# Optimization experiments

Hardware: AMD Instinct MI355X
Metric: run time of the kernel (lower is better)

The kernel has to match this reference:

```python
import jax, jax.numpy as jnp
import numpy as np

D_ENC, D_PRED, D_JOINT, VOCAB = 512, 640, 640, 1024

def setup_inputs() -> dict:
    key = jax.random.key(0)
    ks = jax.random.split(key, 8)
    B, T, U = 8, 200, 50
    s_enc = 1.0 / np.sqrt(D_ENC)
    s_pred = 1.0 / np.sqrt(D_PRED)
    s_joint = 1.0 / np.sqrt(D_JOINT)
    return {
        "encoder_out": jax.random.normal(ks[0], (B, T, D_ENC), jnp.float32),
        "predictor_out": jax.random.normal(ks[1], (B, U, D_PRED), jnp.float32),
        # nn.Linear weights: (out, in), uniform(-1/sqrt(in), 1/sqrt(in))
        "W_enc": jax.random.uniform(ks[2], (D_JOINT, D_ENC), jnp.float32, -s_enc, s_enc),
        "b_enc": jax.random.uniform(ks[3], (D_JOINT,), jnp.float32, -s_enc, s_enc),
        "W_pred": jax.random.uniform(ks[4], (D_JOINT, D_PRED), jnp.float32, -s_pred, s_pred),
        "b_pred": jax.random.uniform(ks[5], (D_JOINT,), jnp.float32, -s_pred, s_pred),
        "W_out": jax.random.uniform(ks[6], (VOCAB, D_JOINT), jnp.float32, -s_joint, s_joint),
        "b_out": jax.random.uniform(ks[7], (VOCAB,), jnp.float32, -s_joint, s_joint),
    }

def reference(encoder_out, predictor_out, W_enc, b_enc, W_pred, b_pred, W_out, b_out):
    # (B,T,d_joint) and (B,U,d_joint) projections
    enc = jnp.einsum('btd,jd->btj', encoder_out, W_enc) + b_enc
    pred = jnp.einsum('bud,jd->buj', predictor_out, W_pred) + b_pred
    # broadcast-add over (T,U), tanh, then output projection -> (B,T,U,V)
    joint = jnp.tanh(enc[:, :, None, :] + pred[:, None, :, :])
    return jnp.einsum('btuj,vj->btuv', joint, W_out) + b_out
```

## Files before the change

kernel.cpp:

```cpp
#include <hip/hip_runtime.h>
#include <hip/hip_bf16.h>
#include <stdint.h>
#include <stddef.h>

#define D_ENC 512
#define D_J   640
#define VOCAB 1024
#define BB    8
#define TT    200
#define UU    50

typedef __bf16 bf16x8 __attribute__((ext_vector_type(8)));
typedef float  f32x4  __attribute__((ext_vector_type(4)));

static __device__ __forceinline__ unsigned f2bf(float x) {
    union { float f; unsigned u; } v; v.f = x;
    unsigned r = v.u + 0x7FFFu + ((v.u >> 16) & 1u);
    return r >> 16;
}
static __device__ __forceinline__ unsigned pk2(float a, float b) {
    return f2bf(a) | (f2bf(b) << 16);
}

static __device__ __forceinline__ float tanh_fast(float x) {
    float ax = __builtin_fabsf(x);
    float e  = __expf(-2.0f * ax);
    float t  = (1.0f - e) * __builtin_amdgcn_rcpf(1.0f + e);
    return __builtin_copysignf(t, x);
}

__global__ void wcvt_kernel(const float* __restrict__ src,
                            unsigned short* __restrict__ dst, int n8) {
    int i = blockIdx.x * blockDim.x + threadIdx.x;
    if (i >= n8) return;
    const float4* s = (const float4*)src + (size_t)i * 2;
    float4 a = s[0], b = s[1];
    uint4 o;
    o.x = pk2(a.x, a.y); o.y = pk2(a.z, a.w);
    o.z = pk2(b.x, b.y); o.w = pk2(b.z, b.w);
    ((uint4*)dst)[i] = o;
}

__global__ void proj_gemm(const float* __restrict__ A, const float* __restrict__ W,
                          const float* __restrict__ bias, float* __restrict__ C,
                          int M, int K) {
    __shared__ __align__(16) unsigned short Alds[64 * 72];
    __shared__ __align__(16) unsigned short Blds[64 * 72];
    const int tid  = threadIdx.x;
    const int lane = tid & 63, w = tid >> 6;
    const int l15  = lane & 15, quad = lane >> 4;
    const int m0 = blockIdx.x * 64, n0 = blockIdx.y * 64;
    const int srow = tid >> 2, sq = tid & 3;

    f32x4 acc[4];
#pragma unroll
    for (int i = 0; i < 4; ++i) acc[i] = (f32x4){0.f, 0.f, 0.f, 0.f};

    const int am = m0 + srow;
    const float* arow = A + (size_t)am * K + sq * 16;
    const float* wrow = W + (size_t)(n0 + srow) * K + sq * 16;
    unsigned short* adst = &Alds[srow * 72 + sq * 16];
    unsigned short* bdst = &Blds[srow * 72 + sq * 16];

    for (int k0 = 0; k0 < K; k0 += 64) {
        uint4 wa0, wa1;
        if (am < M) {
            const float4* p = (const float4*)(arow + k0);
            float4 x0 = p[0], x1 = p[1], x2 = p[2], x3 = p[3];
            wa0.x = pk2(x0.x, x0.y); wa0.y = pk2(x0.z, x0.w);
            wa0.z = pk2(x1.x, x1.y); wa0.w = pk2(x1.z, x1.w);
            wa1.x = pk2(x2.x, x2.y); wa1.y = pk2(x2.z, x2.w);
            wa1.z = pk2(x3.x, x3.y); wa1.w = pk2(x3.z, x3.w);
        } else {
            wa0 = make_uint4(0u, 0u, 0u, 0u); wa1 = wa0;
        }
        uint4 wb0, wb1;
        {
            const float4* p = (const float4*)(wrow + k0);
            float4 x0 = p[0], x1 = p[1], x2 = p[2], x3 = p[3];
            wb0.x = pk2(x0.x, x0.y); wb0.y = pk2(x0.z, x0.w);
            wb0.z = pk2(x1.x, x1.y); wb0.w = pk2(x1.z, x1.w);
            wb1.x = pk2(x2.x, x2.y); wb1.y = pk2(x2.z, x2.w);
            wb1.z = pk2(x3.x, x3.y); wb1.w = pk2(x3.z, x3.w);
        }
        *(uint4*)adst = wa0; *(uint4*)(adst + 8) = wa1;
        *(uint4*)bdst = wb0; *(uint4*)(bdst + 8) = wb1;
        __syncthreads();
#pragma unroll
        for (int ks = 0; ks < 2; ++ks) {
            bf16x8 af = *(const bf16x8*)&Alds[(w * 16 + l15) * 72 + ks * 32 + quad * 8];
#pragma unroll
            for (int nt = 0; nt < 4; ++nt) {
                bf16x8 bf = *(const bf16x8*)&Blds[(nt * 16 + l15) * 72 + ks * 32 + quad * 8];
                acc[nt] = __builtin_amdgcn_mfma_f32_16x16x32_bf16(af, bf, acc[nt], 0, 0, 0);
            }
        }
        __syncthreads();
    }
#pragma unroll
    for (int nt = 0; nt < 4; ++nt) {
        const int n = n0 + nt * 16 + l15;
        const float bo = bias[n];
#pragma unroll
        for (int r = 0; r < 4; ++r) {
            const int mm = m0 + w * 16 + quad * 4 + r;
            if (mm < M) C[(size_t)mm * D_J + n] = acc[nt][r] + bo;
        }
    }
}

#define TANH4(d, e, p)                         \
    d.x = tanh_fast(e.x + p.x);                \
    d.y = tanh_fast(e.y + p.y);                \
    d.z = tanh_fast(e.z + p.z);                \
    d.w = tanh_fast(e.w + p.w);

#define STAGE(dstp, kk)                                      \
    {                                                        \
        const float4* ep = (const float4*)(erow + (kk));     \
        const float4* pp = (const float4*)(prow + (kk));     \
        float4 e0 = ep[0], e1 = ep[1];                       \
        float4 p0 = pp[0], p1 = pp[1];                       \
        float4 t0, t1;                                       \
        TANH4(t0, e0, p0); TANH4(t1, e1, p1);                \
        uint4 s;                                             \
        s.x = pk2(t0.x, t0.y); s.y = pk2(t0.z, t0.w);        \
        s.z = pk2(t1.x, t1.y); s.w = pk2(t1.z, t1.w);        \
        *(uint4*)(dstp) = s;                                 \
    }

__global__ void __launch_bounds__(512, 2)
joint_kernel(const float* __restrict__ encp,
             const float* __restrict__ predp,
             const unsigned short* __restrict__ Wb,
             const float* __restrict__ bout,
             float* __restrict__ out) {
    __shared__ __align__(16) unsigned short Alds[2][64 * 72];
    const int tid  = threadIdx.x;
    const int lane = tid & 63, w = tid >> 6;
    const int l15  = lane & 15, quad = (lane >> 4) & 3;
    const int m0 = blockIdx.x * 64;
    const int n0 = w * 128;
    const int srow = tid >> 3, sq = tid & 7;

    const int m  = m0 + srow;
    const int bt = m / UU;
    const int u  = m - bt * UU;
    const int b  = bt / TT;
    const float* erow = encp  + (size_t)bt * D_J + sq * 8;
    const float* prow = predp + (size_t)(b * UU + u) * D_J + sq * 8;
    const unsigned short* wrow = Wb + (size_t)(n0 + l15) * D_J + quad * 8;
    unsigned short* adst0 = &Alds[0][srow * 72 + sq * 8];
    unsigned short* adst1 = adst0 + 64 * 72;

    f32x4 acc[4][8];
#pragma unroll
    for (int i = 0; i < 4; ++i)
#pragma unroll
        for (int j = 0; j < 8; ++j) acc[i][j] = (f32x4){0.f, 0.f, 0.f, 0.f};

    STAGE(adst0, 0);
    __syncthreads();

    for (int kt = 0; kt < 10; ++kt) {
        const int k0  = kt * 64;
        const int cur = kt & 1;
        if (kt < 9) STAGE(cur ? adst0 : adst1, k0 + 64);

#pragma unroll
        for (int ks = 0; ks < 2; ++ks) {
            uint4 bfr[8];
#pragma unroll
            for (int nt = 0; nt < 8; ++nt)
                bfr[nt] = *(const uint4*)(wrow + (size_t)nt * 16 * D_J + k0 + ks * 32);
            bf16x8 af[4];
#pragma unroll
            for (int mt = 0; mt < 4; ++mt)
                af[mt] = *(const bf16x8*)&Alds[cur][(mt * 16 + l15) * 72 + ks * 32 + quad * 8];
#pragma unroll
            for (int mt = 0; mt < 4; ++mt)
#pragma unroll
                for (int nt = 0; nt < 8; ++nt)
                    acc[mt][nt] = __builtin_amdgcn_mfma_f32_16x16x32_bf16(
                        af[mt], __builtin_bit_cast(bf16x8, bfr[nt]), acc[mt][nt], 0, 0, 0);
        }
        __syncthreads();
    }

#pragma unroll
    for (int nt = 0; nt < 8; ++nt) {
        const int n = n0 + nt * 16 + l15;
        const float bo = bout[n];
#pragma unroll
        for (int mt = 0; mt < 4; ++mt) {
#pragma unroll
            for (int r = 0; r < 4; ++r) {
                const int mm = m0 + mt * 16 + quad * 4 + r;
                out[(size_t)mm * VOCAB + n] = acc[mt][nt][r] + bo;
            }
        }
    }
}

extern "C" void kernel_launch(void* const* d_in, const int* in_sizes, int n_in,
                              void* d_out, int out_size, void* d_ws, size_t ws_size,
                              hipStream_t stream) {
    const float* enc    = (const float*)d_in[0];
    const float* pred   = (const float*)d_in[1];
    const float* W_enc  = (const float*)d_in[2];
    const float* b_enc  = (const float*)d_in[3];
    const float* W_pred = (const float*)d_in[4];
    const float* b_pred = (const float*)d_in[5];
    const float* W_out  = (const float*)d_in[6];
    const float* b_out  = (const float*)d_in[7];
    float* out = (float*)d_out;

    char* ws = (char*)d_ws;
    unsigned short* Wob = (unsigned short*)ws;
    float* encp  = (float*)(ws + 1310720);
    float* predp = (float*)(ws + 1310720 + 4096000);

    wcvt_kernel<<<320, 256, 0, stream>>>(W_out, Wob, 81920);
    proj_gemm<<<dim3(25, 10), 256, 0, stream>>>(enc,  W_enc,  b_enc,  encp,  1600, 512);
    proj_gemm<<<dim3(7, 10),  256, 0, stream>>>(pred, W_pred, b_pred, predp, 400,  640);
    joint_kernel<<<dim3(1250), 512, 0, stream>>>(encp, predp, Wob, b_out, out);
}
```

Measured before the change: 607.7 us.

## Split joint GEMM over vocab blocks with smaller workgroups and nontemporal stores

The joint kernel grid is split four ways along the vocabulary, so each 256-thread block computes a 64x256 output tile with four waves instead of 64x1024 with eight. This cuts accumulator registers per thread and allows more resident blocks, but each block now recomputes the tanh staging of the shared A tile, multiplying that work by four. Output writes switch to nontemporal stores to reduce cache pollution from the large streaming output.

```diff
diff --git a/kernel.cpp b/kernel.cpp
--- a/kernel.cpp
+++ b/kernel.cpp
@@ -115,21 +115,26 @@
     d.z = tanh_fast(e.z + p.z);                \
     d.w = tanh_fast(e.w + p.w);
 
-#define STAGE(dstp, kk)                                      \
+#define STAGE16(dstp, kk)                                    \
     {                                                        \
+        unsigned short* _dst = (dstp);                       \
         const float4* ep = (const float4*)(erow + (kk));     \
         const float4* pp = (const float4*)(prow + (kk));     \
-        float4 e0 = ep[0], e1 = ep[1];                       \
-        float4 p0 = pp[0], p1 = pp[1];                       \
-        float4 t0, t1;                                       \
+        float4 e0 = ep[0], e1 = ep[1], e2 = ep[2], e3 = ep[3]; \
+        float4 p0 = pp[0], p1 = pp[1], p2 = pp[2], p3 = pp[3]; \
+        float4 t0, t1, t2, t3;                               \
         TANH4(t0, e0, p0); TANH4(t1, e1, p1);                \
-        uint4 s;                                             \
-        s.x = pk2(t0.x, t0.y); s.y = pk2(t0.z, t0.w);        \
-        s.z = pk2(t1.x, t1.y); s.w = pk2(t1.z, t1.w);        \
-        *(uint4*)(dstp) = s;                                 \
-    }
-
-__global__ void __launch_bounds__(512, 2)
+        TANH4(t2, e2, p2); TANH4(t3, e3, p3);                \
+        uint4 s0, s1;                                        \
+        s0.x = pk2(t0.x, t0.y); s0.y = pk2(t0.z, t0.w);      \
+        s0.z = pk2(t1.x, t1.y); s0.w = pk2(t1.z, t1.w);      \
+        s1.x = pk2(t2.x, t2.y); s1.y = pk2(t2.z, t2.w);      \
+        s1.z = pk2(t3.x, t3.y); s1.w = pk2(t3.z, t3.w);      \
+        *(uint4*)_dst = s0;                                  \
+        *(uint4*)(_dst + 8) = s1;                            \
+    }
+
+__global__ void __launch_bounds__(256, 3)
 joint_kernel(const float* __restrict__ encp,
              const float* __restrict__ predp,
              const unsigned short* __restrict__ Wb,
@@ -140,38 +145,38 @@
     const int lane = tid & 63, w = tid >> 6;
     const int l15  = lane & 15, quad = (lane >> 4) & 3;
     const int m0 = blockIdx.x * 64;
-    const int n0 = w * 128;
-    const int srow = tid >> 3, sq = tid & 7;
+    const int n0 = blockIdx.y * 256 + w * 64;
+    const int srow = tid >> 2, sq = tid & 3;
 
     const int m  = m0 + srow;
     const int bt = m / UU;
     const int u  = m - bt * UU;
     const int b  = bt / TT;
-    const float* erow = encp  + (size_t)bt * D_J + sq * 8;
-    const float* prow = predp + (size_t)(b * UU + u) * D_J + sq * 8;
+    const float* erow = encp  + (size_t)bt * D_J + sq * 16;
+    const float* prow = predp + (size_t)(b * UU + u) * D_J + sq * 16;
     const unsigned short* wrow = Wb + (size_t)(n0 + l15) * D_J + quad * 8;
-    unsigned short* adst0 = &Alds[0][srow * 72 + sq * 8];
+    unsigned short* adst0 = &Alds[0][srow * 72 + sq * 16];
     unsigned short* adst1 = adst0 + 64 * 72;
 
-    f32x4 acc[4][8];
+    f32x4 acc[4][4];
 #pragma unroll
     for (int i = 0; i < 4; ++i)
 #pragma unroll
-        for (int j = 0; j < 8; ++j) acc[i][j] = (f32x4){0.f, 0.f, 0.f, 0.f};
-
-    STAGE(adst0, 0);
+        for (int j = 0; j < 4; ++j) acc[i][j] = (f32x4){0.f, 0.f, 0.f, 0.f};
+
+    STAGE16(adst0, 0);
     __syncthreads();
 
     for (int kt = 0; kt < 10; ++kt) {
         const int k0  = kt * 64;
         const int cur = kt & 1;
-        if (kt < 9) STAGE(cur ? adst0 : adst1, k0 + 64);
+        if (kt < 9) STAGE16(cur ? adst0 : adst1, k0 + 64);
 
 #pragma unroll
         for (int ks = 0; ks < 2; ++ks) {
-            uint4 bfr[8];
-#pragma unroll
-            for (int nt = 0; nt < 8; ++nt)
+            uint4 bfr[4];
+#pragma unroll
+            for (int nt = 0; nt < 4; ++nt)
                 bfr[nt] = *(const uint4*)(wrow + (size_t)nt * 16 * D_J + k0 + ks * 32);
             bf16x8 af[4];
 #pragma unroll
@@ -180,7 +185,7 @@
 #pragma unroll
             for (int mt = 0; mt < 4; ++mt)
 #pragma unroll
-                for (int nt = 0; nt < 8; ++nt)
+                for (int nt = 0; nt < 4; ++nt)
                     acc[mt][nt] = __builtin_amdgcn_mfma_f32_16x16x32_bf16(
                         af[mt], __builtin_bit_cast(bf16x8, bfr[nt]), acc[mt][nt], 0, 0, 0);
         }
@@ -188,7 +193,7 @@
     }
 
 #pragma unroll
-    for (int nt = 0; nt < 8; ++nt) {
+    for (int nt = 0; nt < 4; ++nt) {
         const int n = n0 + nt * 16 + l15;
         const float bo = bout[n];
 #pragma unroll
@@ -196,7 +201,8 @@
 #pragma unroll
             for (int r = 0; r < 4; ++r) {
                 const int mm = m0 + mt * 16 + quad * 4 + r;
-                out[(size_t)mm * VOCAB + n] = acc[mt][nt][r] + bo;
+                __builtin_nontemporal_store(acc[mt][nt][r] + bo,
+                                            &out[(size_t)mm * VOCAB + n]);
             }
         }
     }
@@ -223,5 +229,5 @@
     wcvt_kernel<<<320, 256, 0, stream>>>(W_out, Wob, 81920);
     proj_gemm<<<dim3(25, 10), 256, 0, stream>>>(enc,  W_enc,  b_enc,  encp,  1600, 512);
     proj_gemm<<<dim3(7, 10),  256, 0, stream>>>(pred, W_pred, b_pred, predp, 400,  640);
-    joint_kernel<<<dim3(1250), 512, 0, stream>>>(encp, predp, Wob, b_out, out);
-}
+    joint_kernel<<<dim3(1250, 4), 256, 0, stream>>>(encp, predp, Wob, b_out, out);
+}
```

Result: no change. 609.8 us (+0.3%).
